# Optimization experiments

Measured on AMD Instinct MI355X. Metric: run time of the kernel, lower is better.

## Reference

```python
import jax, jax.numpy as jnp
import numpy as np

N_NODES = 100000
N_EDGES = 3200000
N_GRAPHS = 125  # 800 nodes per graph
D_IN, D_H1, D_H2, D_OUT = 64, 64, 64, 64


def setup_inputs() -> dict:
    key = jax.random.key(0)
    ks = jax.random.split(key, 9)
    x = jax.random.normal(ks[0], (N_NODES, D_IN), dtype=jnp.float32)
    edge_index = jax.random.randint(ks[1], (2, N_EDGES), 0, N_NODES, dtype=jnp.int32)
    ptr = jnp.arange(0, N_NODES + 1, N_NODES // N_GRAPHS, dtype=jnp.int32)  # [126]
    s1 = 1.0 / np.sqrt(D_IN)
    s2 = 1.0 / np.sqrt(D_H1)
    s3 = 1.0 / np.sqrt(D_H2)
    W1 = jax.random.normal(ks[2], (D_IN, D_H1), jnp.float32) * s1
    b1 = jnp.zeros((D_H1,), jnp.float32)
    W2 = jax.random.normal(ks[3], (D_H1, D_H2), jnp.float32) * s2
    b2 = jnp.zeros((D_H2,), jnp.float32)
    Wf = jax.random.normal(ks[4], (D_H2, D_OUT), jnp.float32) * s3
    bf = jax.random.normal(ks[5], (D_OUT,), jnp.float32) * s3
    return {"x": x, "edge_index": edge_index, "ptr": ptr,
            "W1": W1, "b1": b1, "W2": W2, "b2": b2, "Wf": Wf, "bf": bf}


def _gcn_conv(x, src, dst, deg_inv_sqrt, W, b):
    # PyG GCNConv: h = x @ W; symmetric norm with self-loops; scatter-add; + bias
    h = x @ W                                    # [N, d_out]
    norm = deg_inv_sqrt[src] * deg_inv_sqrt[dst]  # [E]
    msg = h[src] * norm[:, None]                 # [E, d_out] gather + scale
    agg = jax.ops.segment_sum(msg, dst, num_segments=N_NODES)
    # self-loop contribution: norm_ii = deg_inv_sqrt[i]^2
    agg = agg + h * (deg_inv_sqrt ** 2)[:, None]
    return agg + b


def reference(x, edge_index, ptr, W1, b1, W2, b2, Wf, bf):
    src = edge_index[0]
    dst = edge_index[1]
    # degree at target, including the self-loop
    deg = jax.ops.segment_sum(jnp.ones((N_EDGES,), x.dtype), dst,
                              num_segments=N_NODES) + 1.0
    deg_inv_sqrt = jax.lax.rsqrt(deg)

    h = jax.nn.relu(_gcn_conv(x, src, dst, deg_inv_sqrt, W1, b1))
    h = jax.nn.relu(_gcn_conv(h, src, dst, deg_inv_sqrt, W2, b2))
    h = h @ Wf + bf                              # [N, D_OUT]

    # mean aggregation per graph defined by ptr boundaries
    seg = jnp.searchsorted(ptr, jnp.arange(N_NODES, dtype=ptr.dtype),
                           side='right') - 1     # [N] graph id per node
    sums = jax.ops.segment_sum(h, seg, num_segments=N_GRAPHS)  # [G, D_OUT]
    counts = (ptr[1:] - ptr[:-1]).astype(h.dtype)              # [G]
    return sums / counts[:, None]
```

## Files before the change

### kernel.cpp

```cpp
#include <hip/hip_runtime.h>
#include <hip/hip_bf16.h>

#define N_NODES 100000
#define N_EDGES 3200000
#define N_GRAPHS 125
#define D 64
#define NB 800
#define BW 125
#define CAP 5120
#define SC_WGS 256
#define SC_EPW 12500
#define SC_THREADS 1024
#define SC_ITERS 13
#define BUILD_THREADS 512
#define BUILD_ITERS 10

typedef __bf16 bf16x8 __attribute__((ext_vector_type(8)));
typedef float f32x4 __attribute__((ext_vector_type(4)));
typedef float f32x2 __attribute__((ext_vector_type(2)));

__device__ __forceinline__ float bf_lo(unsigned u) { return __uint_as_float(u << 16); }
__device__ __forceinline__ float bf_hi(unsigned u) { return __uint_as_float(u & 0xffff0000u); }
__device__ __forceinline__ f32x2 bf2(unsigned u) {
    f32x2 r;
    r.x = __uint_as_float(u << 16);
    r.y = __uint_as_float(u & 0xffff0000u);
    return r;
}
__device__ __forceinline__ unsigned short f2bf(float f) {
    unsigned u = __float_as_uint(f);
    return (unsigned short)((u + 0x7fffu + ((u >> 16) & 1u)) >> 16);
}


__global__ void bucket_scatter(const int* __restrict__ src, const int* __restrict__ dst,
                               int* __restrict__ bcursor, unsigned* __restrict__ pairs) {
    __shared__ int bins[NB];
    int wg = blockIdx.x, t = threadIdx.x;
    int e0 = wg * SC_EPW;
    if (t < NB) bins[t] = 0;
    __syncthreads();
    unsigned pw[SC_ITERS];
    int      bl[SC_ITERS];
#pragma unroll
    for (int j = 0; j < SC_ITERS; ++j) {
        int o = t + j * SC_THREADS;
        if (o < SC_EPW) {
            int i = e0 + o;
            int s = src[i], d = dst[i];
            int b = d / BW;
            pw[j] = ((unsigned)s << 7) | (unsigned)(d - b * BW);
            bl[j] = b;
            atomicAdd(&bins[b], 1);
        }
    }
    __syncthreads();
    if (t < NB) {
        int c = bins[t];
        bins[t] = t * CAP + (c ? atomicAdd(&bcursor[t], c) : 0);
    }
    __syncthreads();
#pragma unroll
    for (int j = 0; j < SC_ITERS; ++j) {
        int o = t + j * SC_THREADS;
        if (o < SC_EPW) {
            int pos = atomicAdd(&bins[bl[j]], 1);
            pairs[pos] = pw[j];
        }
    }
}

__global__ void bucket_build(const unsigned* __restrict__ pairs, const int* __restrict__ bcursor,
                             int* __restrict__ deg, float* __restrict__ dis,
                             int* __restrict__ row_start, int* __restrict__ csr) {
    __shared__ int h[BW];
    __shared__ int sc[128];
    __shared__ int cur[BW];
    int b = blockIdx.x, t = threadIdx.x;
    int nb = b * BW;
    if (t < BW) h[t] = 0;
    __syncthreads();
    int base = b * CAP, n = bcursor[b];
    unsigned pw[BUILD_ITERS];
#pragma unroll
    for (int j = 0; j < BUILD_ITERS; ++j) {
        int i = t + j * BUILD_THREADS;
        if (i < n) {
            unsigned p = pairs[base + i];
            pw[j] = p;
            atomicAdd(&h[p & 127u], 1);
        }
    }
    __syncthreads();
    int own = 0, own_pad = 0;
    if (t < 128) {
        own = (t < BW) ? h[t] : 0;
        own_pad = (own + 7) & ~7;
        sc[t] = own_pad;
    }
    if (t < BW) {
        deg[nb + t] = own;
        dis[nb + t] = rsqrtf((float)own + 1.0f);
    }
    __syncthreads();
    for (int off = 1; off < 128; off <<= 1) {
        int v = (t >= off && t < 128) ? sc[t - off] : 0;
        __syncthreads();
        if (t < 128) sc[t] += v;
        __syncthreads();
    }
    if (t < BW) {
        int rs = base + sc[t] - own_pad;
        row_start[nb + t] = rs;
        cur[t] = rs;
        for (int k = own; k < own_pad; ++k)
            csr[rs + k] = N_NODES;
    }
    __syncthreads();
#pragma unroll
    for (int j = 0; j < BUILD_ITERS; ++j) {
        int i = t + j * BUILD_THREADS;
        if (i < n) {
            unsigned p = pw[j];
            int pos = atomicAdd(&cur[p & 127u], 1);
            csr[pos] = (int)(p >> 7);
        }
    }
}


__global__ void mfma_gemm(const unsigned short* __restrict__ Xb, const float* __restrict__ W,
                          const float* __restrict__ dis, unsigned short* __restrict__ Y) {
    int lane = threadIdx.x & 63;
    int wid  = (blockIdx.x * blockDim.x + threadIdx.x) >> 6;
    int nwav = (gridDim.x * blockDim.x) >> 6;
    int nl = lane & 15;
    int kq = lane >> 4;
    int kb = kq * 8;
    union BV { unsigned short s[8]; bf16x8 v; } b0[4], b1[4];
#pragma unroll
    for (int nt = 0; nt < 4; ++nt) {
        int nn = nt * 16 + nl;
#pragma unroll
        for (int j = 0; j < 8; ++j) {
            b0[nt].s[j] = f2bf(W[(kb + j) * 64 + nn]);
            b1[nt].s[j] = f2bf(W[(32 + kb + j) * 64 + nn]);
        }
    }
    const uint4* X4 = (const uint4*)Xb;
    for (int t = wid; t < N_NODES / 16; t += nwav) {
        int m0 = t * 16;
        uint4 a0u = X4[(size_t)(m0 + nl) * 8 + kq];
        uint4 a1u = X4[(size_t)(m0 + nl) * 8 + 4 + kq];
        bf16x8 a0 = __builtin_bit_cast(bf16x8, a0u);
        bf16x8 a1 = __builtin_bit_cast(bf16x8, a1u);
        f32x4 acc[4];
#pragma unroll
        for (int nt = 0; nt < 4; ++nt) {
            acc[nt] = (f32x4){0.0f, 0.0f, 0.0f, 0.0f};
            acc[nt] = __builtin_amdgcn_mfma_f32_16x16x32_bf16(a0, b0[nt].v, acc[nt], 0, 0, 0);
            acc[nt] = __builtin_amdgcn_mfma_f32_16x16x32_bf16(a1, b1[nt].v, acc[nt], 0, 0, 0);
        }
        int rbase = m0 + kq * 4;
        float d0 = dis[rbase], d1 = dis[rbase + 1], d2 = dis[rbase + 2], d3 = dis[rbase + 3];
#pragma unroll
        for (int nt = 0; nt < 4; ++nt) {
            int nn = nt * 16 + nl;
            Y[(size_t)(rbase + 0) * 64 + nn] = f2bf(acc[nt][0] * d0);
            Y[(size_t)(rbase + 1) * 64 + nn] = f2bf(acc[nt][1] * d1);
            Y[(size_t)(rbase + 2) * 64 + nn] = f2bf(acc[nt][2] * d2);
            Y[(size_t)(rbase + 3) * 64 + nn] = f2bf(acc[nt][3] * d3);
        }
    }
}

__global__ void mfma_gemm_f32(const float* __restrict__ X, const float* __restrict__ W,
                              const float* __restrict__ dis, unsigned short* __restrict__ Y) {
    int lane = threadIdx.x & 63;
    int wid  = (blockIdx.x * blockDim.x + threadIdx.x) >> 6;
    int nwav = (gridDim.x * blockDim.x) >> 6;
    int nl = lane & 15;
    int kq = lane >> 4;
    int kb = kq * 8;
    union BV { unsigned short s[8]; bf16x8 v; } b0[4], b1[4];
#pragma unroll
    for (int nt = 0; nt < 4; ++nt) {
        int nn = nt * 16 + nl;
#pragma unroll
        for (int j = 0; j < 8; ++j) {
            b0[nt].s[j] = f2bf(W[(kb + j) * 64 + nn]);
            b1[nt].s[j] = f2bf(W[(32 + kb + j) * 64 + nn]);
        }
    }
    const float4* Xf = (const float4*)X;
    for (int t = wid; t < N_NODES / 16; t += nwav) {
        int m0 = t * 16;
        size_t rb = (size_t)(m0 + nl) * 16;
        float4 f0 = Xf[rb + 2 * kq];
        float4 f1 = Xf[rb + 2 * kq + 1];
        float4 f2 = Xf[rb + 8 + 2 * kq];
        float4 f3 = Xf[rb + 8 + 2 * kq + 1];
        union BV av0, av1;
        av0.s[0] = f2bf(f0.x); av0.s[1] = f2bf(f0.y); av0.s[2] = f2bf(f0.z); av0.s[3] = f2bf(f0.w);
        av0.s[4] = f2bf(f1.x); av0.s[5] = f2bf(f1.y); av0.s[6] = f2bf(f1.z); av0.s[7] = f2bf(f1.w);
        av1.s[0] = f2bf(f2.x); av1.s[1] = f2bf(f2.y); av1.s[2] = f2bf(f2.z); av1.s[3] = f2bf(f2.w);
        av1.s[4] = f2bf(f3.x); av1.s[5] = f2bf(f3.y); av1.s[6] = f2bf(f3.z); av1.s[7] = f2bf(f3.w);
        f32x4 acc[4];
#pragma unroll
        for (int nt = 0; nt < 4; ++nt) {
            acc[nt] = (f32x4){0.0f, 0.0f, 0.0f, 0.0f};
            acc[nt] = __builtin_amdgcn_mfma_f32_16x16x32_bf16(av0.v, b0[nt].v, acc[nt], 0, 0, 0);
            acc[nt] = __builtin_amdgcn_mfma_f32_16x16x32_bf16(av1.v, b1[nt].v, acc[nt], 0, 0, 0);
        }
        int rbase = m0 + kq * 4;
        float d0 = dis[rbase], d1 = dis[rbase + 1], d2 = dis[rbase + 2], d3 = dis[rbase + 3];
#pragma unroll
        for (int nt = 0; nt < 4; ++nt) {
            int nn = nt * 16 + nl;
            Y[(size_t)(rbase + 0) * 64 + nn] = f2bf(acc[nt][0] * d0);
            Y[(size_t)(rbase + 1) * 64 + nn] = f2bf(acc[nt][1] * d1);
            Y[(size_t)(rbase + 2) * 64 + nn] = f2bf(acc[nt][2] * d2);
            Y[(size_t)(rbase + 3) * 64 + nn] = f2bf(acc[nt][3] * d3);
        }
    }
}

__global__ void gather_kernel(const unsigned short* __restrict__ Hb, const int* __restrict__ csr,
                              const int* __restrict__ row_start, const int* __restrict__ deg,
                              const float* __restrict__ dis,
                              const float* __restrict__ bias, void* __restrict__ Out,
                              int do_relu, int fuse_pool, float* __restrict__ P) {
    __shared__ float tmp[4][64];
    int v    = (blockIdx.x * blockDim.x + threadIdx.x) >> 6;
    int lane = threadIdx.x & 63;
    int oct  = lane >> 3;
    int l8   = lane & 7;
    int base = row_start[v];
    int n = deg[v];
    float disv = dis[v];
    const uint4* H4 = (const uint4*)Hb;

    f32x2 c0 = {0.f, 0.f}, c1 = {0.f, 0.f}, c2 = {0.f, 0.f}, c3 = {0.f, 0.f};
    if (oct == 0) {
        uint4 hv = H4[((unsigned)v << 3) + (unsigned)l8];
        c0 = bf2(hv.x); c1 = bf2(hv.y); c2 = bf2(hv.z); c3 = bf2(hv.w);
    }

    int groups = (n + 7) >> 3;
    const int* cp = csr + base + oct;
#pragma unroll 4
    for (int g = 0; g < groups; ++g) {
        int ssrc = cp[g << 3];
        uint4 hv = H4[((unsigned)ssrc << 3) + (unsigned)l8];
        c0 += bf2(hv.x); c1 += bf2(hv.y);
        c2 += bf2(hv.z); c3 += bf2(hv.w);
    }
    float a0 = c0.x, a1 = c0.y, a2 = c1.x, a3 = c1.y;
    float a4 = c2.x, a5 = c2.y, a6 = c3.x, a7 = c3.y;
#pragma unroll
    for (int off = 8; off <= 32; off <<= 1) {
        a0 += __shfl_xor(a0, off); a1 += __shfl_xor(a1, off);
        a2 += __shfl_xor(a2, off); a3 += __shfl_xor(a3, off);
        a4 += __shfl_xor(a4, off); a5 += __shfl_xor(a5, off);
        a6 += __shfl_xor(a6, off); a7 += __shfl_xor(a7, off);
    }
    if (oct == 0) {
        float4 blo = ((const float4*)bias)[2 * l8];
        float4 bhi = ((const float4*)bias)[2 * l8 + 1];
        a0 = fmaf(a0, disv, blo.x); a1 = fmaf(a1, disv, blo.y);
        a2 = fmaf(a2, disv, blo.z); a3 = fmaf(a3, disv, blo.w);
        a4 = fmaf(a4, disv, bhi.x); a5 = fmaf(a5, disv, bhi.y);
        a6 = fmaf(a6, disv, bhi.z); a7 = fmaf(a7, disv, bhi.w);
        if (do_relu) {
            a0 = fmaxf(a0, 0.0f); a1 = fmaxf(a1, 0.0f); a2 = fmaxf(a2, 0.0f); a3 = fmaxf(a3, 0.0f);
            a4 = fmaxf(a4, 0.0f); a5 = fmaxf(a5, 0.0f); a6 = fmaxf(a6, 0.0f); a7 = fmaxf(a7, 0.0f);
        }
        if (!fuse_pool) {
            union { unsigned short s[8]; uint4 u; } p;
            p.s[0] = f2bf(a0); p.s[1] = f2bf(a1); p.s[2] = f2bf(a2); p.s[3] = f2bf(a3);
            p.s[4] = f2bf(a4); p.s[5] = f2bf(a5); p.s[6] = f2bf(a6); p.s[7] = f2bf(a7);
            ((uint4*)Out)[((unsigned)v << 3) + (unsigned)l8] = p.u;
        } else {
            float* tr = &tmp[threadIdx.x >> 6][l8 * 8];
            tr[0] = a0; tr[1] = a1; tr[2] = a2; tr[3] = a3;
            tr[4] = a4; tr[5] = a5; tr[6] = a6; tr[7] = a7;
        }
    }
    if (fuse_pool) {
        __syncthreads();
        if (threadIdx.x < 64) {
            int cc = threadIdx.x;
            float s = tmp[0][cc] + tmp[1][cc] + tmp[2][cc] + tmp[3][cc];
            int g = blockIdx.x / 200;
            atomicAdd(&P[g * 64 + cc], s);
        }
    }
}

__global__ void gemm_kernel(const float* __restrict__ X, const float* __restrict__ W,
                            const float* __restrict__ bias, float* __restrict__ Y,
                            int nrows) {
    __shared__ float Ws[64][64];
    for (int i = threadIdx.x; i < 64 * 64; i += 256)
        Ws[i >> 6][i & 63] = W[i];
    __syncthreads();
    int c  = threadIdx.x & 63;
    int rl = threadIdx.x >> 6;
    int r  = blockIdx.x * 4 + rl;
    if (r < nrows) {
        const float* xr = X + (size_t)r * D;
        float dot = 0.0f;
#pragma unroll
        for (int k = 0; k < 64; ++k)
            dot = fmaf(xr[k], Ws[k][c], dot);
        Y[(size_t)r * D + c] = fmaf(dot, 1.0f / 800.0f, bias[c]);
    }
}

extern "C" void kernel_launch(void* const* d_in, const int* in_sizes, int n_in,
                              void* d_out, int out_size, void* d_ws, size_t ws_size,
                              hipStream_t stream) {
    const float* x   = (const float*)d_in[0];
    const int*   ei  = (const int*)d_in[1];
    const int*   src = ei;
    const int*   dst = ei + N_EDGES;
    const float* W1  = (const float*)d_in[3];
    const float* b1  = (const float*)d_in[4];
    const float* W2  = (const float*)d_in[5];
    const float* b2  = (const float*)d_in[6];
    const float* Wf  = (const float*)d_in[7];
    const float* bfp = (const float*)d_in[8];
    float* out = (float*)d_out;

    int*   deg       = (int*)d_ws;
    int*   row_start = deg + 100352;
    int*   bcursor   = row_start + 100352;
    float* P         = (float*)(bcursor + 1024);
    float* dis       = P + 8192;
    int*   csr       = (int*)(dis + 100352);
    float* R         = (float*)(csr + 4096000);
    unsigned short* Ab = (unsigned short*)R;
    unsigned short* Hb = (unsigned short*)(R + 3200064);
    unsigned* pairs  = (unsigned*)(R + 6400128);

    hipMemsetAsync(bcursor, 0, (1024 + 8192) * sizeof(int), stream);
    hipMemsetAsync(Ab + (size_t)N_NODES * D, 0, D * sizeof(unsigned short), stream);
    bucket_scatter<<<SC_WGS, SC_THREADS, 0, stream>>>(src, dst, bcursor, pairs);
    bucket_build<<<NB, BUILD_THREADS, 0, stream>>>(pairs, bcursor, deg, dis, row_start, csr);

    const int grid4 = (N_NODES + 3) / 4;

    mfma_gemm_f32<<<782, 256, 0, stream>>>(x, W1, dis, Ab);
    gather_kernel<<<grid4, 256, 0, stream>>>(Ab, csr, row_start, deg, dis, b1, Hb, 1, 0, nullptr);

    mfma_gemm<<<782, 256, 0, stream>>>(Hb, W2, dis, Ab);
    gather_kernel<<<grid4, 256, 0, stream>>>(Ab, csr, row_start, deg, dis, b2, nullptr, 1, 1, P);

    gemm_kernel<<<(N_GRAPHS + 3) / 4, 256, 0, stream>>>(P, Wf, bfp, out, N_GRAPHS);
}
```

Before: 283.9 us.

## Stage bucket scatter through LDS for coalesced global writes

```diff
diff --git a/kernel.cpp b/kernel.cpp
--- a/kernel.cpp
+++ b/kernel.cpp
@@ -8,10 +8,10 @@
 #define NB 800
 #define BW 125
 #define CAP 5120
-#define SC_WGS 256
-#define SC_EPW 12500
+#define SC_WGS 512
+#define SC_EPW 6250
 #define SC_THREADS 1024
-#define SC_ITERS 13
+#define SC_ITERS 7
 #define BUILD_THREADS 512
 #define BUILD_ITERS 10
 
@@ -35,10 +35,15 @@
 
 __global__ void bucket_scatter(const int* __restrict__ src, const int* __restrict__ dst,
                                int* __restrict__ bcursor, unsigned* __restrict__ pairs) {
-    __shared__ int bins[NB];
+    __shared__ unsigned stage[SC_EPW];
+    __shared__ unsigned short bkt[SC_EPW];
+    __shared__ int hist[NB];
+    __shared__ int sc[SC_THREADS];
+    __shared__ int cursor[NB];
+    __shared__ int goff[NB];
     int wg = blockIdx.x, t = threadIdx.x;
     int e0 = wg * SC_EPW;
-    if (t < NB) bins[t] = 0;
+    if (t < NB) hist[t] = 0;
     __syncthreads();
     unsigned pw[SC_ITERS];
     int      bl[SC_ITERS];
@@ -51,21 +56,42 @@
             int b = d / BW;
             pw[j] = ((unsigned)s << 7) | (unsigned)(d - b * BW);
             bl[j] = b;
-            atomicAdd(&bins[b], 1);
-        }
-    }
-    __syncthreads();
+            atomicAdd(&hist[b], 1);
+        }
+    }
+    __syncthreads();
+    int own = (t < NB) ? hist[t] : 0;
+    sc[t] = own;
+    __syncthreads();
+    for (int off = 1; off < SC_THREADS; off <<= 1) {
+        int v = (t >= off) ? sc[t - off] : 0;
+        __syncthreads();
+        sc[t] += v;
+        __syncthreads();
+    }
     if (t < NB) {
-        int c = bins[t];
-        bins[t] = t * CAP + (c ? atomicAdd(&bcursor[t], c) : 0);
+        int lstart = sc[t] - own;
+        cursor[t] = lstart;
+        int gbase = t * CAP + (own ? atomicAdd(&bcursor[t], own) : 0);
+        goff[t] = gbase - lstart;
     }
     __syncthreads();
 #pragma unroll
     for (int j = 0; j < SC_ITERS; ++j) {
         int o = t + j * SC_THREADS;
         if (o < SC_EPW) {
-            int pos = atomicAdd(&bins[bl[j]], 1);
-            pairs[pos] = pw[j];
+            int pos = atomicAdd(&cursor[bl[j]], 1);
+            stage[pos] = pw[j];
+            bkt[pos] = (unsigned short)bl[j];
+        }
+    }
+    __syncthreads();
+#pragma unroll
+    for (int j = 0; j < SC_ITERS; ++j) {
+        int i = t + j * SC_THREADS;
+        if (i < SC_EPW) {
+            int b = bkt[i];
+            pairs[goff[b] + i] = stage[i];
         }
     }
 }
```

New measurement: 275.3 us. 1.03x faster.
